# Performance work log

Measured on AMD Instinct MI355X. Metric: run time of the kernel, lower is better.

Reference implementation:

```python
import jax, jax.numpy as jnp
import numpy as np

B, S, D, H = 4, 2048, 768, 8
HD = D // H
EPS = 1e-5
NEG = -1e9


def setup_inputs() -> dict:
    key = jax.random.key(0)
    ks = jax.random.split(key, 12)
    s = 1.0 / np.sqrt(D)
    inp = {
        "hidden_states": jax.random.normal(ks[0], (B, S, D), dtype=jnp.float32),
        "anchor_mask": jax.random.bernoulli(ks[1], 0.5, (B, S)),
        "ln_g": jnp.ones((D,), jnp.float32),
        "ln_b": jnp.zeros((D,), jnp.float32),
        "Wq": jax.random.uniform(ks[2], (D, D), jnp.float32, -s, s),
        "bq": jax.random.uniform(ks[3], (D,), jnp.float32, -s, s),
        "Wk": jax.random.uniform(ks[4], (D, D), jnp.float32, -s, s),
        "bk": jax.random.uniform(ks[5], (D,), jnp.float32, -s, s),
        "Wv": jax.random.uniform(ks[6], (D, D), jnp.float32, -s, s),
        "bv": jax.random.uniform(ks[7], (D,), jnp.float32, -s, s),
        "Wo": jax.random.uniform(ks[8], (D, D), jnp.float32, -s, s),
        "bo": jax.random.uniform(ks[9], (D,), jnp.float32, -s, s),
    }
    return inp


def reference(hidden_states, anchor_mask, ln_g, ln_b, Wq, bq, Wk, bk, Wv, bv, Wo, bo):
    # LayerNorm (per-token, so applying to all tokens == applying to gathered anchors)
    mu = jnp.mean(hidden_states, axis=-1, keepdims=True)
    var = jnp.mean(jnp.square(hidden_states - mu), axis=-1, keepdims=True)
    x = (hidden_states - mu) * jax.lax.rsqrt(var + EPS) * ln_g + ln_b

    # QKV projections: torch Linear is x @ W.T + b
    q = (jnp.einsum('bsd,ed->bse', x, Wq) + bq).reshape(B, S, H, HD)
    k = (jnp.einsum('bsd,ed->bse', x, Wk) + bk).reshape(B, S, H, HD)
    v = (jnp.einsum('bsd,ed->bse', x, Wv) + bv).reshape(B, S, H, HD)

    scale = 1.0 / np.sqrt(HD)
    scores = jnp.einsum('bqhd,bkhd->bhqk', q, k) * scale
    # keys restricted to anchor positions (equivalent to the gather)
    key_mask = anchor_mask[:, None, None, :]  # (B,1,1,S)
    scores = jnp.where(key_mask, scores, NEG)
    attn = jax.nn.softmax(scores, axis=-1)  # dropout is identity in eval

    out = jnp.einsum('bhqk,bkhd->bqhd', attn, v).reshape(B, S, D)
    out = jnp.einsum('bsd,ed->bse', out, Wo) + bo
    # scatter back: zeros at non-anchor positions
    return out * anchor_mask[:, :, None].astype(out.dtype)
```

## Files before the change

### kernel.cpp

```cpp
#include <hip/hip_runtime.h>
#include <math.h>

#define S_LEN 2048
#define D_DIM 768
#define NH 8
#define HD 96
#define NTOK 8192

typedef short bf16x8 __attribute__((ext_vector_type(8)));
typedef float f32x4 __attribute__((ext_vector_type(4)));

__device__ __forceinline__ f32x4 mfma16(bf16x8 a, bf16x8 b, f32x4 c) {
    return __builtin_amdgcn_mfma_f32_16x16x32_bf16(a, b, c, 0, 0, 0);
}

__device__ __forceinline__ unsigned short f2bf(float f) {
    unsigned int u = __float_as_uint(f);
    u += 0x7fffu + ((u >> 16) & 1u);
    return (unsigned short)(u >> 16);
}

__device__ __forceinline__ void gl_lds16(const unsigned short* g, unsigned short* l) {
    __builtin_amdgcn_global_load_lds(
        (const __attribute__((address_space(1))) unsigned int*)g,
        (__attribute__((address_space(3))) unsigned int*)l, 16, 0, 0);
}

__global__ __launch_bounds__(256) void prep_kernel(
    const unsigned char* __restrict__ mb, int* __restrict__ idx, int* __restrict__ cnt,
    const float* __restrict__ Wq, const float* __restrict__ Wk,
    const float* __restrict__ Wv, const float* __restrict__ Wo,
    unsigned short* __restrict__ W4b, float* __restrict__ out)
{
    const int bi = blockIdx.x;
    const int t  = threadIdx.x;

    if (bi < 4) {
        __shared__ int red[4];
        __shared__ int warp_tot[4];
        const int b = bi;
        int s = 0;
        for (int i = t; i < NTOK; i += 256) s += (int)mb[i];
        for (int off = 32; off > 0; off >>= 1) s += __shfl_down(s, off, 64);
        if ((t & 63) == 0) red[t >> 6] = s;
        __syncthreads();
        const int total = red[0] + red[1] + red[2] + red[3];
        const int mode = (total > 20000) ? 2 : ((total > 2500) ? 1 : 0);
        const int*   mi = (const int*)mb;
        const float* mf = (const float*)mb;
        const int p0 = t * 8;
        int av = 0, c = 0;
        #pragma unroll
        for (int j = 0; j < 8; ++j) {
            const int g = b * S_LEN + p0 + j;
            bool a;
            if (mode == 2)      a = (mf[g] != 0.0f);
            else if (mode == 1) a = (mb[g] != 0);
            else                a = (mi[g] != 0);
            if (a) { av |= (1 << j); ++c; }
        }
        const int lane = t & 63, w = t >> 6;
        int v = c;
        #pragma unroll
        for (int off = 1; off < 64; off <<= 1) {
            const int u = __shfl_up(v, off, 64);
            if (lane >= off) v += u;
        }
        if (lane == 63) warp_tot[w] = v;
        __syncthreads();
        int wbase = 0;
        for (int i = 0; i < w; ++i) wbase += warp_tot[i];
        int o = wbase + v - c;
        #pragma unroll
        for (int j = 0; j < 8; ++j)
            if (av & (1 << j)) idx[b * S_LEN + (o++)] = p0 + j;
        if (t == 255) cnt[b] = wbase + v;
    } else if (bi < 1156) {
        const int i = bi - 4;
        const int w = i / 288, blk = i % 288;
        const float* src = (w == 0) ? Wq : (w == 1) ? Wk : (w == 2) ? Wv : Wo;
        const int base = (blk * 256 + t) * 8;
        const float4 a = *(const float4*)&src[base];
        const float4 c = *(const float4*)&src[base + 4];
        uint4 u;
        u.x = (unsigned int)f2bf(a.x) | ((unsigned int)f2bf(a.y) << 16);
        u.y = (unsigned int)f2bf(a.z) | ((unsigned int)f2bf(a.w) << 16);
        u.z = (unsigned int)f2bf(c.x) | ((unsigned int)f2bf(c.y) << 16);
        u.w = (unsigned int)f2bf(c.z) | ((unsigned int)f2bf(c.w) << 16);
        *(uint4*)&W4b[(size_t)w * 589824 + base] = u;
    } else {
        const size_t i4 = (size_t)(bi - 1156) * 256 + t;
        float4 z; z.x = z.y = z.z = z.w = 0.0f;
        *(float4*)&out[i4 * 4] = z;
    }
}

__global__ __launch_bounds__(256) void ln_gather_kernel(
    const float* __restrict__ H, const float* __restrict__ g,
    const float* __restrict__ bta, const int* __restrict__ idx,
    const int* __restrict__ cnt, unsigned short* __restrict__ X)
{
    __shared__ float rs[4], rss[4];
    const int slot = blockIdx.x;
    const int b = slot >> 11, r = slot & (S_LEN - 1);
    if (r >= cnt[b]) return;
    const int p = idx[slot];
    const float* hr = H + (size_t)(b * S_LEN + p) * D_DIM;
    unsigned short* xr = X + (size_t)slot * D_DIM;
    const int t = threadIdx.x;
    const float v0 = hr[t], v1 = hr[t + 256], v2 = hr[t + 512];
    float s  = v0 + v1 + v2;
    float ss = v0*v0 + v1*v1 + v2*v2;
    for (int off = 32; off > 0; off >>= 1) {
        s  += __shfl_down(s,  off, 64);
        ss += __shfl_down(ss, off, 64);
    }
    if ((t & 63) == 0) { rs[t >> 6] = s; rss[t >> 6] = ss; }
    __syncthreads();
    const float sum = rs[0] + rs[1] + rs[2] + rs[3];
    const float sq  = rss[0] + rss[1] + rss[2] + rss[3];
    const float mu  = sum * (1.0f / D_DIM);
    const float var = sq * (1.0f / D_DIM) - mu * mu;
    const float rstd = rsqrtf(var + 1e-5f);
    xr[t]       = f2bf((v0 - mu) * rstd * g[t]       + bta[t]);
    xr[t + 256] = f2bf((v1 - mu) * rstd * g[t + 256] + bta[t + 256]);
    xr[t + 512] = f2bf((v2 - mu) * rstd * g[t + 512] + bta[t + 512]);
}

__global__ __launch_bounds__(256) void gemm_bf16(
    const unsigned short* __restrict__ A,
    const unsigned short* __restrict__ W4,
    const float* __restrict__ b0, const float* __restrict__ b1,
    const float* __restrict__ b2,
    const int* __restrict__ cnt, const int* __restrict__ idx,
    unsigned short* __restrict__ Qo, unsigned short* __restrict__ Ko,
    unsigned short* __restrict__ Vo, float* __restrict__ Fo,
    int oproj)
{
    const int z = blockIdx.z;
    const int m0 = blockIdx.y * 128;
    const int b  = m0 >> 11;
    const int rbase = m0 & (S_LEN - 1);
    const int nc = cnt[b];
    if (rbase >= nc) return;
    const int n0 = blockIdx.x * 128;
    const unsigned short* W = W4 + (size_t)z * 589824;
    const float* bias = (z == 0) ? b0 : (z == 1 ? b1 : b2);

    __shared__ unsigned short Al[128 * 32];
    __shared__ unsigned short Bl[128 * 32];

    const int t = threadIdx.x;
    const int srow = t >> 2, sg = t & 3;
    const int ra0 = b * S_LEN + min(rbase + srow,      nc - 1);
    const int ra1 = b * S_LEN + min(rbase + srow + 64, nc - 1);
    const unsigned short* gA0 = A + (size_t)ra0 * 768 + sg * 8;
    const unsigned short* gA1 = A + (size_t)ra1 * 768 + sg * 8;
    const unsigned short* gB0 = W + (size_t)(n0 + srow)      * 768 + sg * 8;
    const unsigned short* gB1 = W + (size_t)(n0 + srow + 64) * 768 + sg * 8;
    unsigned short* lA = Al + t * 8;
    unsigned short* lB = Bl + t * 8;

    const int w = t >> 6, lane = t & 63;
    const int l15 = lane & 15, quad = lane >> 4;
    const int mh = (w & 1) * 64, nh2 = (w >> 1) * 64;

    f32x4 acc[4][4] = {};

    int aoff[4], boff[4];
    #pragma unroll
    for (int i = 0; i < 4; ++i) {
        aoff[i] = (mh  + i * 16 + l15) * 32 + quad * 8;
        boff[i] = (nh2 + i * 16 + l15) * 32 + quad * 8;
    }

    for (int k0 = 0; k0 < 768; k0 += 32) {
        __syncthreads();
        gl_lds16(gA0 + k0, lA);
        gl_lds16(gA1 + k0, lA + 2048);
        gl_lds16(gB0 + k0, lB);
        gl_lds16(gB1 + k0, lB + 2048);
        __syncthreads();
        bf16x8 af[4], bfr[4];
        #pragma unroll
        for (int i = 0; i < 4; ++i) af[i]  = *(const bf16x8*)(Al + aoff[i]);
        #pragma unroll
        for (int i = 0; i < 4; ++i) bfr[i] = *(const bf16x8*)(Bl + boff[i]);
        #pragma unroll
        for (int ms = 0; ms < 4; ++ms)
            #pragma unroll
            for (int ns = 0; ns < 4; ++ns)
                acc[ms][ns] = mfma16(af[ms], bfr[ns], acc[ms][ns]);
    }

    if (!oproj) {
        if (z < 2) {
            unsigned short* O = (z == 0) ? Qo : Ko;
            #pragma unroll
            for (int ns = 0; ns < 4; ++ns) {
                const int n = n0 + nh2 + ns * 16 + l15;
                const float bv = bias[n];
                #pragma unroll
                for (int ms = 0; ms < 4; ++ms) {
                    const int ml = mh + ms * 16 + quad * 4;
                    #pragma unroll
                    for (int r = 0; r < 4; ++r) {
                        const int slot = b * S_LEN + rbase + ml + r;
                        O[(size_t)slot * 768 + n] = f2bf(acc[ms][ns][r] + bv);
                    }
                }
            }
        } else {
            #pragma unroll
            for (int ns = 0; ns < 4; ++ns) {
                const int n = n0 + nh2 + ns * 16 + l15;
                const float bv = bias[n];
                #pragma unroll
                for (int ms = 0; ms < 4; ++ms) {
                    const int ml = mh + ms * 16 + quad * 4;
                    const unsigned short h0 = f2bf(acc[ms][ns][0] + bv);
                    const unsigned short h1 = f2bf(acc[ms][ns][1] + bv);
                    const unsigned short h2 = f2bf(acc[ms][ns][2] + bv);
                    const unsigned short h3 = f2bf(acc[ms][ns][3] + bv);
                    uint2 u;
                    u.x = (unsigned int)h0 | ((unsigned int)h1 << 16);
                    u.y = (unsigned int)h2 | ((unsigned int)h3 << 16);
                    *(uint2*)&Vo[((size_t)b * 768 + n) * S_LEN + rbase + ml] = u;
                }
            }
        }
    } else {
        #pragma unroll
        for (int ns = 0; ns < 4; ++ns) {
            const int n = n0 + nh2 + ns * 16 + l15;
            const float bv = bias[n];
            #pragma unroll
            for (int ms = 0; ms < 4; ++ms) {
                const int ml = mh + ms * 16 + quad * 4;
                #pragma unroll
                for (int r = 0; r < 4; ++r) {
                    const int rloc = rbase + ml + r;
                    if (rloc < nc) {
                        const int orow = b * S_LEN + idx[b * S_LEN + rloc];
                        Fo[(size_t)orow * 768 + n] = acc[ms][ns][r] + bv;
                    }
                }
            }
        }
    }
}

__global__ __launch_bounds__(256) void attn_mfma(
    const unsigned short* __restrict__ Q,
    const unsigned short* __restrict__ K,
    const unsigned short* __restrict__ Vt,
    const int* __restrict__ cnt,
    unsigned short* __restrict__ O)
{
    const int q0 = blockIdx.x * 64;
    const int h  = blockIdx.y;
    const int b  = blockIdx.z;
    const int nk = cnt[b];
    if (q0 >= nk) return;

    __shared__ unsigned short SB[6144 + 6144 + 4 * 1152];
    unsigned short* Kl = SB;
    unsigned short* Vl = SB + 6144;

    const int t = threadIdx.x, w = t >> 6, lane = t & 63;
    const int l15 = lane & 15, quad = lane >> 4;
    const int qw = q0 + w * 16;
    const int bS = b * S_LEN;
    const float CE = 0.14724459f;

    const unsigned short* gsrc[6];
    int gdst[6], gstep[6];
    #pragma unroll
    for (int r = 0; r < 6; ++r) {
        const int g = r * 256 + t;
        if (g < 768) {
            const int g16 = g / 192, rem = g % 192;
            const int dseg = rem >> 4, lr = rem & 15;
            gsrc[r] = K + (size_t)(bS + g16 * 16 + lr) * 768 + h * 96 + dseg * 8;
            gstep[r] = 64 * 768;
            gdst[r] = g * 8;
        } else {
            const int j = g - 768;
            const int dg = j >> 7, rem = j & 127;
            const int kseg = rem >> 4, lr = rem & 15;
            gsrc[r] = Vt + ((size_t)b * 768 + h * 96 + dg * 16 + lr) * 2048 + kseg * 8;
            gstep[r] = 64;
            gdst[r] = 6144 + j * 8;
        }
    }

    const unsigned short* qrow = Q + (size_t)(bS + qw + l15) * 768 + h * 96 + quad * 8;
    bf16x8 qf[3];
    qf[0] = *(const bf16x8*)(qrow);
    qf[1] = *(const bf16x8*)(qrow + 32);
    qf[2] = *(const bf16x8*)(qrow + 64);

    unsigned short* Pw = SB + 12288 + w * 1152;
    float lsum = 0.0f;
    f32x4 oacc[6] = {};

    const int kts = (nk + 63) >> 6;
    for (int kt = 0; kt < kts; ++kt) {
        const int k0 = kt * 64;
        __syncthreads();
        #pragma unroll
        for (int r = 0; r < 6; ++r)
            gl_lds16(gsrc[r] + (size_t)kt * gstep[r], SB + gdst[r]);
        __syncthreads();

        const int lim = nk - k0;
        #pragma unroll
        for (int s = 0; s < 4; ++s) {
            f32x4 sa = {};
            #pragma unroll
            for (int ks = 0; ks < 3; ++ks) {
                const bf16x8 kf = *(const bf16x8*)(Kl + (s * 192 + (quad + ks * 4) * 16 + l15) * 8);
                sa = mfma16(kf, qf[ks], sa);
            }
            unsigned short pk[4];
            #pragma unroll
            for (int r = 0; r < 4; ++r) {
                float p = exp2f(sa[r] * CE);
                p = (s * 16 + quad * 4 + r < lim) ? p : 0.0f;
                lsum += p;
                pk[r] = f2bf(p);
            }
            uint2 u;
            u.x = (unsigned int)pk[0] | ((unsigned int)pk[1] << 16);
            u.y = (unsigned int)pk[2] | ((unsigned int)pk[3] << 16);
            *(uint2*)&Pw[l15 * 72 + s * 16 + quad * 4] = u;
        }

        const bf16x8 pb0 = *(const bf16x8*)(Pw + l15 * 72 + quad * 8);
        const bf16x8 pb1 = *(const bf16x8*)(Pw + l15 * 72 + 32 + quad * 8);

        #pragma unroll
        for (int dt = 0; dt < 6; ++dt) {
            const bf16x8 v0f = *(const bf16x8*)(Vl + (dt * 128 + quad * 16 + l15) * 8);
            const bf16x8 v1f = *(const bf16x8*)(Vl + (dt * 128 + (quad + 4) * 16 + l15) * 8);
            oacc[dt] = mfma16(v0f, pb0, oacc[dt]);
            oacc[dt] = mfma16(v1f, pb1, oacc[dt]);
        }
    }

    lsum += __shfl_xor(lsum, 16);
    lsum += __shfl_xor(lsum, 32);

    const int qi = qw + l15;
    if (qi < nk) {
        const float rl = 1.0f / lsum;
        unsigned short* og = O + (size_t)(bS + qi) * 768 + h * 96;
        #pragma unroll
        for (int dt = 0; dt < 6; ++dt) {
            const unsigned short o0 = f2bf(oacc[dt][0] * rl);
            const unsigned short o1 = f2bf(oacc[dt][1] * rl);
            const unsigned short o2 = f2bf(oacc[dt][2] * rl);
            const unsigned short o3 = f2bf(oacc[dt][3] * rl);
            uint2 u;
            u.x = (unsigned int)o0 | ((unsigned int)o1 << 16);
            u.y = (unsigned int)o2 | ((unsigned int)o3 << 16);
            *(uint2*)&og[dt * 16 + quad * 4] = u;
        }
    }
}

extern "C" void kernel_launch(void* const* d_in, const int* in_sizes, int n_in,
                              void* d_out, int out_size, void* d_ws, size_t ws_size,
                              hipStream_t stream)
{
    const float* hs  = (const float*)d_in[0];
    const unsigned char* am = (const unsigned char*)d_in[1];
    const float* lng = (const float*)d_in[2];
    const float* lnb = (const float*)d_in[3];
    const float* Wq  = (const float*)d_in[4];
    const float* bq  = (const float*)d_in[5];
    const float* Wk  = (const float*)d_in[6];
    const float* bk  = (const float*)d_in[7];
    const float* Wv  = (const float*)d_in[8];
    const float* bv  = (const float*)d_in[9];
    const float* Wo  = (const float*)d_in[10];
    const float* bo  = (const float*)d_in[11];

    char* ws = (char*)d_ws;
    const size_t BUF = (size_t)NTOK * 768 * 2;
    int* idx = (int*)ws;
    int* cnt = (int*)(ws + 32768);
    unsigned short* xb  = (unsigned short*)(ws + 65536);
    unsigned short* Qb  = (unsigned short*)(ws + 65536 + BUF);
    unsigned short* Kb  = (unsigned short*)(ws + 65536 + 2 * BUF);
    unsigned short* Vtb = (unsigned short*)(ws + 65536 + 3 * BUF);
    unsigned short* Ob  = (unsigned short*)(ws + 65536 + 4 * BUF);
    unsigned short* W4b = (unsigned short*)(ws + 65536 + 5 * BUF);
    float* out = (float*)d_out;

    prep_kernel<<<dim3(2692), dim3(256), 0, stream>>>(
        am, idx, cnt, Wq, Wk, Wv, Wo, W4b, out);

    ln_gather_kernel<<<dim3(NTOK), dim3(256), 0, stream>>>(hs, lng, lnb, idx, cnt, xb);

    gemm_bf16<<<dim3(6, 64, 3), dim3(256), 0, stream>>>(
        xb, W4b, bq, bk, bv, cnt, idx, Qb, Kb, Vtb, nullptr, 0);

    attn_mfma<<<dim3(32, NH, 4), dim3(256), 0, stream>>>(Qb, Kb, Vtb, cnt, Ob);

    gemm_bf16<<<dim3(6, 64, 1), dim3(256), 0, stream>>>(
        Ob, W4b + (size_t)3 * 589824, bo, bo, bo, cnt, idx,
        nullptr, nullptr, nullptr, out, 1);
}
```

Baseline: 232.6 us.

## Double-buffer LDS tiles in projection GEMM and attention kernels

Both the QKV/O projection GEMM and the attention kernel now use two LDS buffers. The next K-slice or key/value tile is issued with global_load_lds before computing on the current buffer, so global-to-LDS transfer overlaps the MFMA work. This also drops one of the two barriers per iteration. In exchange, LDS use doubles: the attention block grows to about 59 KB, which may cut how many blocks fit per CU and limit the latency hiding that occupancy provided.

```diff
diff --git a/kernel.cpp b/kernel.cpp
--- a/kernel.cpp
+++ b/kernel.cpp
@@ -147,8 +147,8 @@
     const unsigned short* W = W4 + (size_t)z * 589824;
     const float* bias = (z == 0) ? b0 : (z == 1 ? b1 : b2);
 
-    __shared__ unsigned short Al[128 * 32];
-    __shared__ unsigned short Bl[128 * 32];
+    __shared__ unsigned short Al[2][4096];
+    __shared__ unsigned short Bl[2][4096];
 
     const int t = threadIdx.x;
     const int srow = t >> 2, sg = t & 3;
@@ -158,8 +158,6 @@
     const unsigned short* gA1 = A + (size_t)ra1 * 768 + sg * 8;
     const unsigned short* gB0 = W + (size_t)(n0 + srow)      * 768 + sg * 8;
     const unsigned short* gB1 = W + (size_t)(n0 + srow + 64) * 768 + sg * 8;
-    unsigned short* lA = Al + t * 8;
-    unsigned short* lB = Bl + t * 8;
 
     const int w = t >> 6, lane = t & 63;
     const int l15 = lane & 15, quad = lane >> 4;
@@ -174,23 +172,29 @@
         boff[i] = (nh2 + i * 16 + l15) * 32 + quad * 8;
     }
 
-    for (int k0 = 0; k0 < 768; k0 += 32) {
-        __syncthreads();
-        gl_lds16(gA0 + k0, lA);
-        gl_lds16(gA1 + k0, lA + 2048);
-        gl_lds16(gB0 + k0, lB);
-        gl_lds16(gB1 + k0, lB + 2048);
-        __syncthreads();
+    auto stage = [&](int k0, int par) {
+        gl_lds16(gA0 + k0, &Al[par][t * 8]);
+        gl_lds16(gA1 + k0, &Al[par][2048 + t * 8]);
+        gl_lds16(gB0 + k0, &Bl[par][t * 8]);
+        gl_lds16(gB1 + k0, &Bl[par][2048 + t * 8]);
+    };
+
+    stage(0, 0);
+    __syncthreads();
+    for (int it = 0; it < 24; ++it) {
+        const int par = it & 1;
+        if (it + 1 < 24) stage((it + 1) * 32, par ^ 1);
         bf16x8 af[4], bfr[4];
         #pragma unroll
-        for (int i = 0; i < 4; ++i) af[i]  = *(const bf16x8*)(Al + aoff[i]);
-        #pragma unroll
-        for (int i = 0; i < 4; ++i) bfr[i] = *(const bf16x8*)(Bl + boff[i]);
+        for (int i = 0; i < 4; ++i) af[i]  = *(const bf16x8*)(&Al[par][aoff[i]]);
+        #pragma unroll
+        for (int i = 0; i < 4; ++i) bfr[i] = *(const bf16x8*)(&Bl[par][boff[i]]);
         #pragma unroll
         for (int ms = 0; ms < 4; ++ms)
             #pragma unroll
             for (int ns = 0; ns < 4; ++ns)
                 acc[ms][ns] = mfma16(af[ms], bfr[ns], acc[ms][ns]);
+        __syncthreads();
     }
 
     if (!oproj) {
@@ -263,9 +267,7 @@
     const int nk = cnt[b];
     if (q0 >= nk) return;
 
-    __shared__ unsigned short SB[6144 + 6144 + 4 * 1152];
-    unsigned short* Kl = SB;
-    unsigned short* Vl = SB + 6144;
+    __shared__ unsigned short SB[24576 + 4608];
 
     const int t = threadIdx.x, w = t >> 6, lane = t & 63;
     const int l15 = lane & 15, quad = lane >> 4;
@@ -300,18 +302,26 @@
     qf[1] = *(const bf16x8*)(qrow + 32);
     qf[2] = *(const bf16x8*)(qrow + 64);
 
-    unsigned short* Pw = SB + 12288 + w * 1152;
+    unsigned short* Pw = SB + 24576 + w * 1152;
     float lsum = 0.0f;
     f32x4 oacc[6] = {};
 
     const int kts = (nk + 63) >> 6;
+
+    auto stage = [&](int kt, int par) {
+        #pragma unroll
+        for (int r = 0; r < 6; ++r)
+            gl_lds16(gsrc[r] + (size_t)kt * gstep[r], SB + par * 12288 + gdst[r]);
+    };
+
+    stage(0, 0);
+    __syncthreads();
     for (int kt = 0; kt < kts; ++kt) {
+        const int par = kt & 1;
+        if (kt + 1 < kts) stage(kt + 1, par ^ 1);
+        const unsigned short* Kl = SB + par * 12288;
+        const unsigned short* Vl = Kl + 6144;
         const int k0 = kt * 64;
-        __syncthreads();
-        #pragma unroll
-        for (int r = 0; r < 6; ++r)
-            gl_lds16(gsrc[r] + (size_t)kt * gstep[r], SB + gdst[r]);
-        __syncthreads();
 
         const int lim = nk - k0;
         #pragma unroll
@@ -346,6 +356,7 @@
             oacc[dt] = mfma16(v0f, pb0, oacc[dt]);
             oacc[dt] = mfma16(v1f, pb1, oacc[dt]);
         }
+        __syncthreads();
     }
 
     lsum += __shfl_xor(lsum, 16);
```

Result: slower. 251.5 us (+8.1%).

## Split attention key range across two blocks and combine partials in a separate kernel

Applied to the files above, without the earlier changes.

The attention kernel now splits each query block's key tiles into two halves, one per grid slice, doubling the number of launched blocks. Each half writes unnormalized fp32 output accumulators and row sums to workspace, and a new combine kernel adds the two halves, normalizes and writes bf16 output. This is meant to fix under-occupancy, since only about half the query blocks do work when roughly half the tokens are anchors. The cost is an extra kernel launch and fp32 partial-result traffic through global memory. The combine is only correct because the softmax does not subtract a running maximum.

```diff
diff --git a/kernel.cpp b/kernel.cpp
--- a/kernel.cpp
+++ b/kernel.cpp
@@ -6,6 +6,7 @@
 #define NH 8
 #define HD 96
 #define NTOK 8192
+#define QSTRIDE 1536
 
 typedef short bf16x8 __attribute__((ext_vector_type(8)));
 typedef float f32x4 __attribute__((ext_vector_type(4)));
@@ -250,18 +251,26 @@
     }
 }
 
-__global__ __launch_bounds__(256) void attn_mfma(
+__global__ __launch_bounds__(256) void attn_split(
     const unsigned short* __restrict__ Q,
     const unsigned short* __restrict__ K,
     const unsigned short* __restrict__ Vt,
     const int* __restrict__ cnt,
-    unsigned short* __restrict__ O)
+    float* __restrict__ Op,
+    float* __restrict__ Lp)
 {
     const int q0 = blockIdx.x * 64;
     const int h  = blockIdx.y;
-    const int b  = blockIdx.z;
+    const int z  = blockIdx.z;
+    const int b  = z >> 1, half = z & 1;
     const int nk = cnt[b];
     if (q0 >= nk) return;
+    const int zh = z * 8 + h;
+
+    const int kts = (nk + 63) >> 6;
+    const int ht  = (kts + 1) >> 1;
+    const int kt0 = half ? ht : 0;
+    const int kt1 = half ? kts : ht;
 
     __shared__ unsigned short SB[6144 + 6144 + 4 * 1152];
     unsigned short* Kl = SB;
@@ -304,14 +313,13 @@
     float lsum = 0.0f;
     f32x4 oacc[6] = {};
 
-    const int kts = (nk + 63) >> 6;
-    for (int kt = 0; kt < kts; ++kt) {
-        const int k0 = kt * 64;
+    for (int kt = kt0; kt < kt1; ++kt) {
         __syncthreads();
         #pragma unroll
         for (int r = 0; r < 6; ++r)
             gl_lds16(gsrc[r] + (size_t)kt * gstep[r], SB + gdst[r]);
         __syncthreads();
+        const int k0 = kt * 64;
 
         const int lim = nk - k0;
         #pragma unroll
@@ -351,21 +359,62 @@
     lsum += __shfl_xor(lsum, 16);
     lsum += __shfl_xor(lsum, 32);
 
-    const int qi = qw + l15;
-    if (qi < nk) {
-        const float rl = 1.0f / lsum;
-        unsigned short* og = O + (size_t)(bS + qi) * 768 + h * 96;
-        #pragma unroll
-        for (int dt = 0; dt < 6; ++dt) {
-            const unsigned short o0 = f2bf(oacc[dt][0] * rl);
-            const unsigned short o1 = f2bf(oacc[dt][1] * rl);
-            const unsigned short o2 = f2bf(oacc[dt][2] * rl);
-            const unsigned short o3 = f2bf(oacc[dt][3] * rl);
-            uint2 u;
-            u.x = (unsigned int)o0 | ((unsigned int)o1 << 16);
-            u.y = (unsigned int)o2 | ((unsigned int)o3 << 16);
-            *(uint2*)&og[dt * 16 + quad * 4] = u;
-        }
+    __syncthreads();
+    float* T = (float*)SB + w * 1552;
+    #pragma unroll
+    for (int dt = 0; dt < 6; ++dt)
+        #pragma unroll
+        for (int r = 0; r < 4; ++r)
+            T[l15 * 97 + dt * 16 + quad * 4 + r] = oacc[dt][r];
+    if (quad == 0 && qw + l15 < nk)
+        Lp[(size_t)zh * QSTRIDE + qw + l15] = lsum;
+
+    const int ql = lane >> 2, ck = lane & 3;
+    if (qw + ql < nk) {
+        float* dst = Op + ((size_t)zh * QSTRIDE + qw + ql) * 96 + ck * 24;
+        #pragma unroll
+        for (int i = 0; i < 6; ++i) {
+            float4 v;
+            v.x = T[ql * 97 + ck * 24 + i * 4 + 0];
+            v.y = T[ql * 97 + ck * 24 + i * 4 + 1];
+            v.z = T[ql * 97 + ck * 24 + i * 4 + 2];
+            v.w = T[ql * 97 + ck * 24 + i * 4 + 3];
+            *(float4*)(dst + i * 4) = v;
+        }
+    }
+}
+
+__global__ __launch_bounds__(256) void comb_kernel(
+    const float* __restrict__ Op, const float* __restrict__ Lp,
+    const int* __restrict__ cnt, unsigned short* __restrict__ Ob)
+{
+    const int q0 = blockIdx.x * 64;
+    const int h  = blockIdx.y;
+    const int b  = blockIdx.z;
+    const int nk = cnt[b];
+    if (q0 >= nk) return;
+    const int t = threadIdx.x;
+    const int ql = t >> 2, ck = t & 3;
+    const int q = q0 + ql;
+    if (q >= nk) return;
+    const int zh0 = (b * 2) * 8 + h, zh1 = zh0 + 8;
+    const float L = Lp[(size_t)zh0 * QSTRIDE + q] + Lp[(size_t)zh1 * QSTRIDE + q];
+    const float rl = 1.0f / L;
+    const float* p0 = Op + ((size_t)zh0 * QSTRIDE + q) * 96 + ck * 24;
+    const float* p1 = Op + ((size_t)zh1 * QSTRIDE + q) * 96 + ck * 24;
+    unsigned short* og = Ob + (size_t)(b * S_LEN + q) * 768 + h * 96 + ck * 24;
+    #pragma unroll
+    for (int i = 0; i < 6; ++i) {
+        const float4 a = *(const float4*)(p0 + i * 4);
+        const float4 c = *(const float4*)(p1 + i * 4);
+        const unsigned short h0 = f2bf((a.x + c.x) * rl);
+        const unsigned short h1 = f2bf((a.y + c.y) * rl);
+        const unsigned short h2 = f2bf((a.z + c.z) * rl);
+        const unsigned short h3 = f2bf((a.w + c.w) * rl);
+        uint2 u;
+        u.x = (unsigned int)h0 | ((unsigned int)h1 << 16);
+        u.y = (unsigned int)h2 | ((unsigned int)h3 << 16);
+        *(uint2*)(og + i * 4) = u;
     }
 }
 
@@ -394,8 +443,10 @@
     unsigned short* Qb  = (unsigned short*)(ws + 65536 + BUF);
     unsigned short* Kb  = (unsigned short*)(ws + 65536 + 2 * BUF);
     unsigned short* Vtb = (unsigned short*)(ws + 65536 + 3 * BUF);
-    unsigned short* Ob  = (unsigned short*)(ws + 65536 + 4 * BUF);
-    unsigned short* W4b = (unsigned short*)(ws + 65536 + 5 * BUF);
+    unsigned short* W4b = (unsigned short*)(ws + 65536 + 4 * BUF);
+    float* Op = (float*)(ws + 65536 + 4 * BUF + 4718592);
+    float* Lp = Op + (size_t)64 * QSTRIDE * 96;
+    unsigned short* Ob = xb;
     float* out = (float*)d_out;
 
     prep_kernel<<<dim3(2692), dim3(256), 0, stream>>>(
@@ -406,7 +457,9 @@
     gemm_bf16<<<dim3(6, 64, 3), dim3(256), 0, stream>>>(
         xb, W4b, bq, bk, bv, cnt, idx, Qb, Kb, Vtb, nullptr, 0);
 
-    attn_mfma<<<dim3(32, NH, 4), dim3(256), 0, stream>>>(Qb, Kb, Vtb, cnt, Ob);
+    attn_split<<<dim3(32, NH, 8), dim3(256), 0, stream>>>(Qb, Kb, Vtb, cnt, Op, Lp);
+
+    comb_kernel<<<dim3(32, NH, 4), dim3(256), 0, stream>>>(Op, Lp, cnt, Ob);
 
     gemm_bf16<<<dim3(6, 64, 1), dim3(256), 0, stream>>>(
         Ob, W4b + (size_t)3 * 589824, bo, bo, bo, cnt, idx,
```

New measurement: 247.4 us. 6.4% more time.

## Write K and V in pre-tiled LDS layout so attention loads are contiguous

Applied to the files above, without the earlier changes.

The QKV projection epilogue now writes K and V straight into a per-(batch, head) tiled layout that matches the attention kernel's LDS tile arrangement. The attention kernel can then fetch each 64-key tile with contiguous 16-byte global-to-LDS loads instead of gathering strided rows. The attention output buffer also reuses the LN input buffer to save workspace. The K epilogue now does scattered 2-byte stores, which may slow the GEMM in exchange for cheaper attention-side loads.

```diff
diff --git a/kernel.cpp b/kernel.cpp
--- a/kernel.cpp
+++ b/kernel.cpp
@@ -25,6 +25,9 @@
         (const __attribute__((address_space(1))) unsigned int*)g,
         (__attribute__((address_space(3))) unsigned int*)l, 16, 0, 0);
 }
+
+#define TILE_SHORTS 6144
+#define BH_SHORTS   196608
 
 __global__ __launch_bounds__(256) void prep_kernel(
     const unsigned char* __restrict__ mb, int* __restrict__ idx, int* __restrict__ cnt,
@@ -133,8 +136,8 @@
     const float* __restrict__ b0, const float* __restrict__ b1,
     const float* __restrict__ b2,
     const int* __restrict__ cnt, const int* __restrict__ idx,
-    unsigned short* __restrict__ Qo, unsigned short* __restrict__ Ko,
-    unsigned short* __restrict__ Vo, float* __restrict__ Fo,
+    unsigned short* __restrict__ Qo, unsigned short* __restrict__ Kp,
+    unsigned short* __restrict__ Vp, float* __restrict__ Fo,
     int oproj)
 {
     const int z = blockIdx.z;
@@ -194,8 +197,7 @@
     }
 
     if (!oproj) {
-        if (z < 2) {
-            unsigned short* O = (z == 0) ? Qo : Ko;
+        if (z == 0) {
             #pragma unroll
             for (int ns = 0; ns < 4; ++ns) {
                 const int n = n0 + nh2 + ns * 16 + l15;
@@ -206,18 +208,46 @@
                     #pragma unroll
                     for (int r = 0; r < 4; ++r) {
                         const int slot = b * S_LEN + rbase + ml + r;
-                        O[(size_t)slot * 768 + n] = f2bf(acc[ms][ns][r] + bv);
+                        Qo[(size_t)slot * 768 + n] = f2bf(acc[ms][ns][r] + bv);
                     }
                 }
             }
-        } else {
+        } else if (z == 1) {
             #pragma unroll
             for (int ns = 0; ns < 4; ++ns) {
                 const int n = n0 + nh2 + ns * 16 + l15;
+                const int h = n / 96, d = n - h * 96;
                 const float bv = bias[n];
+                unsigned short* base = Kp + (size_t)(b * 8 + h) * BH_SHORTS;
+                const int dseg = d >> 3, dlo = d & 7;
                 #pragma unroll
                 for (int ms = 0; ms < 4; ++ms) {
                     const int ml = mh + ms * 16 + quad * 4;
+                    #pragma unroll
+                    for (int r = 0; r < 4; ++r) {
+                        const int tok = rbase + ml + r;
+                        const int kt = tok >> 6, tk = tok & 63;
+                        const int g16 = tk >> 4, lr = tk & 15;
+                        base[(size_t)kt * TILE_SHORTS +
+                             (g16 * 192 + dseg * 16 + lr) * 8 + dlo] =
+                            f2bf(acc[ms][ns][r] + bv);
+                    }
+                }
+            }
+        } else {
+            #pragma unroll
+            for (int ns = 0; ns < 4; ++ns) {
+                const int n = n0 + nh2 + ns * 16 + l15;
+                const int h = n / 96, d = n - h * 96;
+                const float bv = bias[n];
+                unsigned short* base = Vp + (size_t)(b * 8 + h) * BH_SHORTS;
+                const int dg = d >> 4, l16 = d & 15;
+                #pragma unroll
+                for (int ms = 0; ms < 4; ++ms) {
+                    const int ml = mh + ms * 16 + quad * 4;
+                    const int k = rbase + ml;
+                    const int kt = k >> 6, tk = k & 63;
+                    const int kseg = tk >> 3, klo = tk & 7;
                     const unsigned short h0 = f2bf(acc[ms][ns][0] + bv);
                     const unsigned short h1 = f2bf(acc[ms][ns][1] + bv);
                     const unsigned short h2 = f2bf(acc[ms][ns][2] + bv);
@@ -225,7 +255,8 @@
                     uint2 u;
                     u.x = (unsigned int)h0 | ((unsigned int)h1 << 16);
                     u.y = (unsigned int)h2 | ((unsigned int)h3 << 16);
-                    *(uint2*)&Vo[((size_t)b * 768 + n) * S_LEN + rbase + ml] = u;
+                    *(uint2*)&base[(size_t)kt * TILE_SHORTS +
+                                   (dg * 128 + kseg * 16 + l16) * 8 + klo] = u;
                 }
             }
         }
@@ -252,8 +283,8 @@
 
 __global__ __launch_bounds__(256) void attn_mfma(
     const unsigned short* __restrict__ Q,
-    const unsigned short* __restrict__ K,
-    const unsigned short* __restrict__ Vt,
+    const unsigned short* __restrict__ Kp,
+    const unsigned short* __restrict__ Vp,
     const int* __restrict__ cnt,
     unsigned short* __restrict__ O)
 {
@@ -273,26 +304,8 @@
     const int bS = b * S_LEN;
     const float CE = 0.14724459f;
 
-    const unsigned short* gsrc[6];
-    int gdst[6], gstep[6];
-    #pragma unroll
-    for (int r = 0; r < 6; ++r) {
-        const int g = r * 256 + t;
-        if (g < 768) {
-            const int g16 = g / 192, rem = g % 192;
-            const int dseg = rem >> 4, lr = rem & 15;
-            gsrc[r] = K + (size_t)(bS + g16 * 16 + lr) * 768 + h * 96 + dseg * 8;
-            gstep[r] = 64 * 768;
-            gdst[r] = g * 8;
-        } else {
-            const int j = g - 768;
-            const int dg = j >> 7, rem = j & 127;
-            const int kseg = rem >> 4, lr = rem & 15;
-            gsrc[r] = Vt + ((size_t)b * 768 + h * 96 + dg * 16 + lr) * 2048 + kseg * 8;
-            gstep[r] = 64;
-            gdst[r] = 6144 + j * 8;
-        }
-    }
+    const unsigned short* Kbh = Kp + (size_t)(b * 8 + h) * BH_SHORTS + t * 8;
+    const unsigned short* Vbh = Vp + (size_t)(b * 8 + h) * BH_SHORTS + t * 8;
 
     const unsigned short* qrow = Q + (size_t)(bS + qw + l15) * 768 + h * 96 + quad * 8;
     bf16x8 qf[3];
@@ -306,12 +319,15 @@
 
     const int kts = (nk + 63) >> 6;
     for (int kt = 0; kt < kts; ++kt) {
+        const size_t tb = (size_t)kt * TILE_SHORTS;
+        __syncthreads();
+        #pragma unroll
+        for (int r = 0; r < 3; ++r) {
+            gl_lds16(Kbh + tb + r * 2048, Kl + r * 2048 + t * 8);
+            gl_lds16(Vbh + tb + r * 2048, Vl + r * 2048 + t * 8);
+        }
+        __syncthreads();
         const int k0 = kt * 64;
-        __syncthreads();
-        #pragma unroll
-        for (int r = 0; r < 6; ++r)
-            gl_lds16(gsrc[r] + (size_t)kt * gstep[r], SB + gdst[r]);
-        __syncthreads();
 
         const int lim = nk - k0;
         #pragma unroll
@@ -392,10 +408,10 @@
     int* cnt = (int*)(ws + 32768);
     unsigned short* xb  = (unsigned short*)(ws + 65536);
     unsigned short* Qb  = (unsigned short*)(ws + 65536 + BUF);
-    unsigned short* Kb  = (unsigned short*)(ws + 65536 + 2 * BUF);
-    unsigned short* Vtb = (unsigned short*)(ws + 65536 + 3 * BUF);
-    unsigned short* Ob  = (unsigned short*)(ws + 65536 + 4 * BUF);
-    unsigned short* W4b = (unsigned short*)(ws + 65536 + 5 * BUF);
+    unsigned short* Kpb = (unsigned short*)(ws + 65536 + 2 * BUF);
+    unsigned short* Vpb = (unsigned short*)(ws + 65536 + 3 * BUF);
+    unsigned short* W4b = (unsigned short*)(ws + 65536 + 4 * BUF);
+    unsigned short* Ob  = xb;
     float* out = (float*)d_out;
 
     prep_kernel<<<dim3(2692), dim3(256), 0, stream>>>(
@@ -404,9 +420,9 @@
     ln_gather_kernel<<<dim3(NTOK), dim3(256), 0, stream>>>(hs, lng, lnb, idx, cnt, xb);
 
     gemm_bf16<<<dim3(6, 64, 3), dim3(256), 0, stream>>>(
-        xb, W4b, bq, bk, bv, cnt, idx, Qb, Kb, Vtb, nullptr, 0);
-
-    attn_mfma<<<dim3(32, NH, 4), dim3(256), 0, stream>>>(Qb, Kb, Vtb, cnt, Ob);
+        xb, W4b, bq, bk, bv, cnt, idx, Qb, Kpb, Vpb, nullptr, 0);
+
+    attn_mfma<<<dim3(32, NH, 4), dim3(256), 0, stream>>>(Qb, Kpb, Vpb, cnt, Ob);
 
     gemm_bf16<<<dim3(6, 64, 1), dim3(256), 0, stream>>>(
         Ob, W4b + (size_t)3 * 589824, bo, bo, bo, cnt, idx,
```

New measurement: 223.2 us. 1.04x faster.
